# Kernel tuning notes

Measured on AMD Instinct MI355X. Metric: run time of the kernel, lower is better.

The kernel has to match this reference:

```python
import jax, jax.numpy as jnp
import numpy as np

N_HEAD = 16
D_HEAD = 64
D_LATENT = 32
BLOCK_SIZE = 2048


def rope_cache(dim, max_seq_len, theta=10000.0):
    inv_freq = 1.0 / (theta ** (jnp.arange(0, dim, 2, dtype=jnp.float32) / dim))
    t = jnp.arange(max_seq_len, dtype=jnp.float32)
    freqs = jnp.einsum('i,j->ij', t, inv_freq)        # [T, dim/2]
    emb = jnp.concatenate([freqs, freqs], axis=-1)    # [T, dim]
    return jnp.cos(emb), jnp.sin(emb)


def apply_rope(x, cos, sin):
    # x: [B, H, T, C]; interleaved-pair rotation as in the torch module
    B, H, T, C = x.shape
    c = cos[:T][None, None]
    s = sin[:T][None, None]
    x1 = x[..., 0::2]
    x2 = x[..., 1::2]
    rotated = jnp.stack((-x2, x1), axis=-1).reshape(B, H, T, C)
    return x * c + rotated * s


def setup_inputs() -> dict:
    key = jax.random.key(0)
    ks = jax.random.split(key, 7)
    sd = 0.02
    return {
        'x':   jax.random.normal(ks[0], (2, 2048, 1024), dtype=jnp.float32),
        'Wq':  jax.random.normal(ks[1], (1024, 1024), dtype=jnp.float32) * sd,
        'Wk':  jax.random.normal(ks[2], (512, 1024), dtype=jnp.float32) * sd,
        'Wv':  jax.random.normal(ks[3], (512, 1024), dtype=jnp.float32) * sd,
        'Wku': jax.random.normal(ks[4], (64, 32), dtype=jnp.float32) * sd,
        'Wvu': jax.random.normal(ks[5], (64, 32), dtype=jnp.float32) * sd,
        'Wc':  jax.random.normal(ks[6], (1024, 1024), dtype=jnp.float32) * sd,
    }


def reference(x, Wq, Wk, Wv, Wku, Wvu, Wc):
    B, T, C = x.shape
    H, Dh, Dl = N_HEAD, D_HEAD, D_LATENT

    # latent KV (compressed cache entries)
    k_lat = (x @ Wk.T).reshape(B, T, H, Dl)   # [B,T,H,Dl]
    v_lat = (x @ Wv.T).reshape(B, T, H, Dl)

    # q and up-projected k/v -> [B,H,T,Dh]
    q = (x @ Wq.T).reshape(B, T, H, Dh).transpose(0, 2, 1, 3)
    k = jnp.einsum('bthl,dl->bhtd', k_lat, Wku)
    v = jnp.einsum('bthl,dl->bhtd', v_lat, Wvu)

    cos, sin = rope_cache(Dh, BLOCK_SIZE)
    q = apply_rope(q, cos, sin)
    k = apply_rope(k, cos, sin)

    scale = 1.0 / jnp.sqrt(jnp.asarray(Dh, dtype=x.dtype))
    att = jnp.einsum('bhqd,bhkd->bhqk', q, k) * scale   # [B,H,T,T]
    causal = jnp.tril(jnp.ones((T, T), dtype=bool))
    att = jnp.where(causal[None, None], att, -jnp.inf)
    att = jax.nn.softmax(att, axis=-1)

    y = jnp.einsum('bhqk,bhkd->bhqd', att, v)           # [B,H,T,Dh]
    y = y.transpose(0, 2, 1, 3).reshape(B, T, C) @ Wc.T  # [B,T,C]
    return y, k_lat, v_lat
```

## Files before the change

kernel.cpp:

```cpp
#include <hip/hip_runtime.h>
#include <math.h>

#define NHEAD  16
#define DHEAD  64
#define DLAT   32
#define TSEQ   2048
#define NBATCH 2
#define CDIM   1024
#define MROWS  (NBATCH*TSEQ)

typedef __attribute__((ext_vector_type(8))) short bf16x8;
typedef __attribute__((ext_vector_type(4))) short bf16x4;
typedef __attribute__((ext_vector_type(4))) float f32x4;

#define AS1 __attribute__((address_space(1)))
#define AS3 __attribute__((address_space(3)))

__device__ __forceinline__ unsigned short f2bf(float f) {
    union { float f; unsigned u; } v; v.f = f;
    unsigned r = v.u + 0x7fff + ((v.u >> 16) & 1);
    return (unsigned short)(r >> 16);
}

__device__ __forceinline__ unsigned pk2(float lo, float hi) {
    return (unsigned)f2bf(lo) | ((unsigned)f2bf(hi) << 16);
}

__device__ __forceinline__ unsigned pack_trunc(float hi, float lo) {
    return __builtin_amdgcn_perm(__float_as_uint(hi), __float_as_uint(lo), 0x07060302u);
}

__device__ __forceinline__ void gld_lds16(const unsigned short* g, unsigned short* l) {
    __builtin_amdgcn_global_load_lds((const AS1 void*)g, (AS3 void*)l, 16, 0, 0);
}

__device__ __forceinline__ f32x4 mfma_16x16x16_bf16(bf16x4 a, bf16x4 b, f32x4 c) {
#if __has_builtin(__builtin_amdgcn_mfma_f32_16x16x16bf16_1k)
    return __builtin_amdgcn_mfma_f32_16x16x16bf16_1k(a, b, c, 0, 0, 0);
#else
    asm volatile("v_mfma_f32_16x16x16_bf16 %0, %1, %2, %0\n\ts_nop 4"
                 : "+v"(c) : "v"(a), "v"(b));
    return c;
#endif
}

__global__ __launch_bounds__(256) void cvt_all(
        const float* __restrict__ x,  const float* __restrict__ wq,
        const float* __restrict__ wk, const float* __restrict__ wv,
        const float* __restrict__ wc, const float* __restrict__ wku,
        const float* __restrict__ wvu,
        unsigned short* __restrict__ xb, unsigned short* __restrict__ wall) {
    int i = (blockIdx.x * 256 + threadIdx.x) * 4;
    const float* src; unsigned short* dst; int off;
    if      (i < 4194304) { src = x;   dst = xb;             off = 0;       }
    else if (i < 5242880) { src = wq;  dst = wall;           off = 4194304; }
    else if (i < 5767168) { src = wk;  dst = wall + 1048576; off = 5242880; }
    else if (i < 6291456) { src = wv;  dst = wall + 1572864; off = 5767168; }
    else if (i < 7340032) { src = wc;  dst = wall + 2097152; off = 6291456; }
    else if (i < 7342080) { src = wku; dst = wall + 3145728; off = 7340032; }
    else                  { src = wvu; dst = wall + 3147776; off = 7342080; }
    float4 v = *(const float4*)(src + (i - off));
    ushort4 o = { f2bf(v.x), f2bf(v.y), f2bf(v.z), f2bf(v.w) };
    *(ushort4*)(dst + (i - off)) = o;
}

__device__ __forceinline__ void gemm_core(
        const unsigned short* __restrict__ A, const unsigned short* __restrict__ W,
        int K, int bm, int bn, unsigned short* As, unsigned short* Bs,
        f32x4 (&acc)[4][4]) {
    const int tid = threadIdx.x;
    const int w = tid >> 6, lane = tid & 63;
    const int quad = lane >> 4, l16 = lane & 15;
    const int wm = (w >> 1) * 64, wn = (w & 1) * 64;

    const int lr = lane >> 2;
    const int le = (lane & 3) * 8;
    const unsigned short* Ag0 = A + (size_t)(bm + w*32 + lr) * K + le;
    const unsigned short* Wg0 = W + (size_t)(bn + w*32 + lr) * K + le;
    unsigned short* AsD0 = &As[(w*32 +  0) * 32];
    unsigned short* AsD1 = &As[(w*32 + 16) * 32];
    unsigned short* BsD0 = &Bs[(w*32 +  0) * 32];
    unsigned short* BsD1 = &Bs[(w*32 + 16) * 32];

    for (int k0 = 0; k0 < K; k0 += 32) {
        gld_lds16(Ag0 + k0,                AsD0);
        gld_lds16(Ag0 + k0 + (size_t)16*K, AsD1);
        gld_lds16(Wg0 + k0,                BsD0);
        gld_lds16(Wg0 + k0 + (size_t)16*K, BsD1);
        __syncthreads();
        bf16x8 af[4], bf[4];
        #pragma unroll
        for (int t = 0; t < 4; ++t)
            af[t] = *(const bf16x8*)&As[(wm + t*16 + l16)*32 + quad*8];
        #pragma unroll
        for (int c = 0; c < 4; ++c)
            bf[c] = *(const bf16x8*)&Bs[(wn + c*16 + l16)*32 + quad*8];
        #pragma unroll
        for (int t = 0; t < 4; ++t)
            #pragma unroll
            for (int c = 0; c < 4; ++c)
                acc[t][c] = __builtin_amdgcn_mfma_f32_16x16x32_bf16(af[t], bf[c], acc[t][c], 0, 0, 0);
        __syncthreads();
    }
}

__global__ __launch_bounds__(256) void gemm_proj(
        const unsigned short* __restrict__ A, const unsigned short* __restrict__ W,
        float* __restrict__ qproj, float* __restrict__ okl, float* __restrict__ ovl,
        int K) {
    __shared__ unsigned short As[128*32];
    __shared__ unsigned short Bs[128*32];
    const int bm = blockIdx.y * 128, bn = blockIdx.x * 128;
    f32x4 acc[4][4] = {};
    gemm_core(A, W, K, bm, bn, As, Bs, acc);

    const int tid = threadIdx.x;
    const int w = tid >> 6, lane = tid & 63;
    const int quad = lane >> 4, l16 = lane & 15;
    const int wm = (w >> 1) * 64, wn = (w & 1) * 64;

    float* base; int ldo;
    if (bn < 1024)      { base = qproj + bn;        ldo = 1024; }
    else if (bn < 1536) { base = okl + (bn - 1024); ldo = 512;  }
    else                { base = ovl + (bn - 1536); ldo = 512;  }

    #pragma unroll
    for (int t = 0; t < 4; ++t)
        #pragma unroll
        for (int c = 0; c < 4; ++c)
            #pragma unroll
            for (int r = 0; r < 4; ++r) {
                int row = bm + wm + t*16 + quad*4 + r;
                int col = wn + c*16 + l16;
                base[(size_t)row * ldo + col] = acc[t][c][r];
            }
}

__global__ __launch_bounds__(256) void gemm_out(
        const unsigned short* __restrict__ A, const unsigned short* __restrict__ W,
        float* __restrict__ O, int N, int K) {
    __shared__ unsigned short As[128*32];
    __shared__ unsigned short Bs[128*32];
    const int bm = blockIdx.y * 128, bn = blockIdx.x * 128;
    f32x4 acc[4][4] = {};
    gemm_core(A, W, K, bm, bn, As, Bs, acc);

    const int tid = threadIdx.x;
    const int w = tid >> 6, lane = tid & 63;
    const int quad = lane >> 4, l16 = lane & 15;
    const int wm = (w >> 1) * 64, wn = (w & 1) * 64;
    #pragma unroll
    for (int t = 0; t < 4; ++t)
        #pragma unroll
        for (int c = 0; c < 4; ++c)
            #pragma unroll
            for (int r = 0; r < 4; ++r) {
                int row = bm + wm + t*16 + quad*4 + r;
                int col = bn + wn + c*16 + l16;
                O[(size_t)row * N + col] = acc[t][c][r];
            }
}

#define QSCALE 0.18033688011112042f
__global__ __launch_bounds__(256) void latup(
        const float* __restrict__ qproj, const float* __restrict__ klat,
        const float* __restrict__ vlat,
        const unsigned short* __restrict__ wkub, const unsigned short* __restrict__ wvub,
        unsigned short* __restrict__ qb, unsigned short* __restrict__ kb,
        unsigned short* __restrict__ vt) {
    __shared__ __attribute__((aligned(16))) unsigned short ksh[4][16][72];
    __shared__ __attribute__((aligned(16))) unsigned short qsh[4][16][72];
    __shared__ __attribute__((aligned(16))) unsigned short vsh[4][64][24];

    const int bh = blockIdx.y, b = bh >> 4, h = bh & 15;
    const int tid = threadIdx.x, w = tid >> 6, lane = tid & 63;
    const int quad = lane >> 4, l16 = lane & 15;
    const int tw = blockIdx.x * 64 + w * 16;
    const int t  = tw + l16;

    const float* klp = klat + ((size_t)(b*TSEQ + t))*(NHEAD*DLAT) + h*DLAT + quad*8;
    const float* vlp = vlat + ((size_t)(b*TSEQ + t))*(NHEAD*DLAT) + h*DLAT + quad*8;
    float4 kA = *(const float4*)klp, kB = *(const float4*)(klp + 4);
    float4 vA = *(const float4*)vlp, vB = *(const float4*)(vlp + 4);

    bf16x8 xk[4], xv[4];
    #pragma unroll
    for (int c = 0; c < 4; ++c) {
        xk[c] = *(const bf16x8*)&wkub[(c*16 + l16)*DLAT + quad*8];
        xv[c] = *(const bf16x8*)&wvub[(c*16 + l16)*DLAT + quad*8];
    }

    union { bf16x8 v; unsigned u[4]; } yk, yv;
    yk.u[0] = pk2(kA.x, kA.y); yk.u[1] = pk2(kA.z, kA.w);
    yk.u[2] = pk2(kB.x, kB.y); yk.u[3] = pk2(kB.z, kB.w);
    yv.u[0] = pk2(vA.x, vA.y); yv.u[1] = pk2(vA.z, vA.w);
    yv.u[2] = pk2(vB.x, vB.y); yv.u[3] = pk2(vB.z, vB.w);

    f32x4 aK[4], aV[4];
    #pragma unroll
    for (int c = 0; c < 4; ++c) {
        f32x4 z = {0.f, 0.f, 0.f, 0.f};
        aK[c] = __builtin_amdgcn_mfma_f32_16x16x32_bf16(xk[c], yk.v, z, 0, 0, 0);
        aV[c] = __builtin_amdgcn_mfma_f32_16x16x32_bf16(xv[c], yv.v, z, 0, 0, 0);
    }

    float C0[4], S0[4], C1[4], S1[4];
    const float tf = (float)t;
    #pragma unroll
    for (int j = 0; j < 4; ++j) {
        float f0 = (float)(quad*4 + j);
        __sincosf(tf * __expf(-f0 * 0.28782313662425572f),          &S0[j], &C0[j]);
        __sincosf(tf * __expf(-(f0 + 16.f) * 0.28782313662425572f), &S1[j], &C1[j]);
    }

    const float* qrow = qproj + ((size_t)(b*TSEQ + t))*CDIM + h*DHEAD;
    #pragma unroll
    for (int c = 0; c < 4; ++c) {
        const float* Cs = (c & 1) ? C1 : C0;
        const float* Ss = (c & 1) ? S1 : S0;
        float a0 = aK[c][0], a1 = aK[c][1], a2 = aK[c][2], a3 = aK[c][3];
        unsigned kw0 = pk2(a0*Cs[0] - a1*Ss[0], a1*Cs[1] + a0*Ss[1]);
        unsigned kw1 = pk2(a2*Cs[2] - a3*Ss[2], a3*Cs[3] + a2*Ss[3]);
        *(uint2*)&ksh[w][l16][c*16 + quad*4] = make_uint2(kw0, kw1);

        float4 qv = *(const float4*)(qrow + c*16 + quad*4);
        unsigned qw0 = pk2((qv.x*Cs[0] - qv.y*Ss[0])*QSCALE, (qv.y*Cs[1] + qv.x*Ss[1])*QSCALE);
        unsigned qw1 = pk2((qv.z*Cs[2] - qv.w*Ss[2])*QSCALE, (qv.w*Cs[3] + qv.z*Ss[3])*QSCALE);
        *(uint2*)&qsh[w][l16][c*16 + quad*4] = make_uint2(qw0, qw1);

        vsh[w][c*16 + quad*4 + 0][l16] = f2bf(aV[c][0]);
        vsh[w][c*16 + quad*4 + 1][l16] = f2bf(aV[c][1]);
        vsh[w][c*16 + quad*4 + 2][l16] = f2bf(aV[c][2]);
        vsh[w][c*16 + quad*4 + 3][l16] = f2bf(aV[c][3]);
    }

    __asm__ __volatile__("s_waitcnt lgkmcnt(0)" ::: "memory");

    const int ro = lane >> 2, co = (lane & 3) * 16;
    size_t go = ((size_t)bh*TSEQ + tw + ro)*DHEAD + co;
    int4 k0o = *(const int4*)&ksh[w][ro][co];
    int4 k1o = *(const int4*)&ksh[w][ro][co + 8];
    *(int4*)&kb[go]     = k0o;
    *(int4*)&kb[go + 8] = k1o;
    int4 q0o = *(const int4*)&qsh[w][ro][co];
    int4 q1o = *(const int4*)&qsh[w][ro][co + 8];
    *(int4*)&qb[go]     = q0o;
    *(int4*)&qb[go + 8] = q1o;

    size_t vo = ((size_t)bh*DHEAD + lane)*TSEQ + tw;
    int4 v0o = *(const int4*)&vsh[w][lane][0];
    int4 v1o = *(const int4*)&vsh[w][lane][8];
    *(int4*)&vt[vo]     = v0o;
    *(int4*)&vt[vo + 8] = v1o;
}

__global__ __launch_bounds__(256, 2) void flash_attn(
        const unsigned short* __restrict__ qb, const unsigned short* __restrict__ kb,
        const unsigned short* __restrict__ vtb, unsigned short* __restrict__ yatt) {
    const int bh = blockIdx.x;
    const int b = bh >> 4, h = bh & 15;

    __shared__ unsigned short Ks[2][128][64];
    __shared__ unsigned short VTs[2][64][128];

    const int tid  = threadIdx.x;
    const int wq   = tid >> 6;
    const int lane = tid & 63;
    const int quad = lane >> 4;
    const int l16  = lane & 15;

    const unsigned short* Kbase = kb  + (size_t)bh * TSEQ * DHEAD;
    const unsigned short* Vbase = vtb + (size_t)bh * DHEAD * TSEQ;

    const int kr8 = lane >> 3, kcp = lane & 7;
    const int kcl = (kcp ^ kr8) * 8;
    const int vr4 = lane >> 4, vcp = lane & 15;

    const int kx0 = (quad ^ (l16 & 7)) * 8;
    const int kx1 = ((quad + 4) ^ (l16 & 7)) * 8;
    const int vq = (quad >> 1), vodd = (quad & 1) * 4;

    for (int half = 0; half < 2; ++half) {
        const int qt = half ? (31 - (int)blockIdx.y) : (int)blockIdx.y;
        const int n128 = (qt + 2) >> 1;

        const unsigned short* qbase =
            qb + ((size_t)bh*TSEQ + qt*64 + wq*16 + l16) * DHEAD + quad*8;
        bf16x8 qB0 = *(const bf16x8*)qbase;
        bf16x8 qB1 = *(const bf16x8*)(qbase + 32);

        f32x4 oacc[4] = {};
        float m_run = -1e30f, l_run = 0.f;

        __syncthreads();
        #pragma unroll
        for (int i = 0; i < 4; ++i) {
            gld_lds16(Kbase + (size_t)(wq*32 + i*8 + kr8)*DHEAD + kcl,
                      &Ks[0][wq*32 + i*8][0]);
            int vcl = (vcp ^ ((i*4 + vr4) & 15)) * 8;
            gld_lds16(Vbase + (size_t)(wq*16 + i*4 + vr4)*TSEQ + vcl,
                      &VTs[0][wq*16 + i*4][0]);
        }
        __syncthreads();

        for (int j = 0; j < n128; ++j) {
            const int buf = j & 1;
            if (j + 1 < n128) {
                const int kc = (j + 1) * 128;
                #pragma unroll
                for (int i = 0; i < 4; ++i) {
                    gld_lds16(Kbase + (size_t)(kc + wq*32 + i*8 + kr8)*DHEAD + kcl,
                              &Ks[buf^1][wq*32 + i*8][0]);
                    int vcl = (vcp ^ ((i*4 + vr4) & 15)) * 8;
                    gld_lds16(Vbase + (size_t)(wq*16 + i*4 + vr4)*TSEQ + kc + vcl,
                              &VTs[buf^1][wq*16 + i*4][0]);
                }
            }

            f32x4 sacc[8];
            __builtin_amdgcn_s_setprio(1);
            #pragma unroll
            for (int c = 0; c < 8; ++c) {
                bf16x8 ak0 = *(const bf16x8*)&Ks[buf][c*16 + l16][kx0];
                bf16x8 ak1 = *(const bf16x8*)&Ks[buf][c*16 + l16][kx1];
                f32x4 z = {0.f, 0.f, 0.f, 0.f};
                z = __builtin_amdgcn_mfma_f32_16x16x32_bf16(ak0, qB0, z, 0, 0, 0);
                z = __builtin_amdgcn_mfma_f32_16x16x32_bf16(ak1, qB1, z, 0, 0, 0);
                sacc[c] = z;
            }
            __builtin_amdgcn_s_setprio(0);
            if (j == n128 - 1) {
                #pragma unroll
                for (int c = 0; c < 8; ++c)
                    #pragma unroll
                    for (int r = 0; r < 4; ++r)
                        if (j*128 + c*16 + quad*4 + r > qt*64 + wq*16 + l16)
                            sacc[c][r] = -1e30f;
            }

            float mx = -1e30f;
            #pragma unroll
            for (int c = 0; c < 8; ++c)
                #pragma unroll
                for (int r = 0; r < 4; ++r) mx = fmaxf(mx, sacc[c][r]);
            mx = fmaxf(mx, __shfl_xor(mx, 16, 64));
            mx = fmaxf(mx, __shfl_xor(mx, 32, 64));
            if (!__all(mx <= m_run + 8.f)) {
                float mn = fmaxf(m_run, mx);
                float alpha = __builtin_exp2f(m_run - mn);
                m_run = mn;
                l_run *= alpha;
                #pragma unroll
                for (int c = 0; c < 4; ++c)
                    #pragma unroll
                    for (int r = 0; r < 4; ++r) oacc[c][r] *= alpha;
            }
            float ls = 0.f;
            #pragma unroll
            for (int c = 0; c < 8; ++c)
                #pragma unroll
                for (int r = 0; r < 4; ++r) {
                    float p = __builtin_exp2f(sacc[c][r] - m_run);
                    sacc[c][r] = p;
                    ls += p;
                }
            ls += __shfl_xor(ls, 16, 64);
            ls += __shfl_xor(ls, 32, 64);
            l_run += ls;

            __builtin_amdgcn_s_setprio(1);
            #pragma unroll
            for (int c = 0; c < 8; ++c) {
                union { bf16x4 v; unsigned u[2]; } bP;
                bP.u[0] = pack_trunc(sacc[c][1], sacc[c][0]);
                bP.u[1] = pack_trunc(sacc[c][3], sacc[c][2]);
                const int vcol = ((2*c + vq) ^ l16) * 8 + vodd;
                #pragma unroll
                for (int dc = 0; dc < 4; ++dc) {
                    bf16x4 av = *(const bf16x4*)&VTs[buf][dc*16 + l16][vcol];
                    oacc[dc] = mfma_16x16x16_bf16(av, bP.v, oacc[dc]);
                }
            }
            __builtin_amdgcn_s_setprio(0);

            __syncthreads();
        }

        float invl = 1.0f / l_run;
        unsigned short* Wt = &Ks[0][0][0] + wq * (16*72);
        #pragma unroll
        for (int c = 0; c < 4; ++c)
            #pragma unroll
            for (int r = 0; r < 4; ++r)
                Wt[(size_t)l16*72 + c*16 + quad*4 + r] = f2bf(oacc[c][r] * invl);
        __asm__ __volatile__("" ::: "memory");
        #pragma unroll
        for (int p = 0; p < 2; ++p) {
            int row = p*8 + (lane >> 3);
            int d0 = (lane & 7) * 8;
            int4 val = *(const int4*)&Wt[row*72 + d0];
            int tg = qt*64 + wq*16 + row;
            *(int4*)&yatt[((size_t)(b*TSEQ + tg))*CDIM + h*DHEAD + d0] = val;
        }
    }
}

extern "C" void kernel_launch(void* const* d_in, const int* in_sizes, int n_in,
                              void* d_out, int out_size, void* d_ws, size_t ws_size,
                              hipStream_t stream) {
    const float* x   = (const float*)d_in[0];
    const float* Wq  = (const float*)d_in[1];
    const float* Wk  = (const float*)d_in[2];
    const float* Wv  = (const float*)d_in[3];
    const float* Wku = (const float*)d_in[4];
    const float* Wvu = (const float*)d_in[5];
    const float* Wc  = (const float*)d_in[6];

    float* out_y  = (float*)d_out;
    float* out_kl = out_y  + (size_t)MROWS * CDIM;
    float* out_vl = out_kl + (size_t)MROWS * NHEAD*DLAT;

    float* qproj = (float*)d_ws;
    unsigned short* xb   = (unsigned short*)(qproj + (size_t)MROWS*CDIM);
    unsigned short* qb   = xb  + (size_t)MROWS*CDIM;
    unsigned short* kb   = qb  + (size_t)MROWS*CDIM;
    unsigned short* vt   = kb  + (size_t)MROWS*CDIM;
    unsigned short* wall = vt  + (size_t)MROWS*CDIM;
    unsigned short* wcb  = wall + (size_t)2048*CDIM;
    unsigned short* wkub = wall + 3145728;
    unsigned short* wvub = wall + 3147776;
    unsigned short* yatt = (unsigned short*)qproj;

    cvt_all<<<7172, 256, 0, stream>>>(x, Wq, Wk, Wv, Wc, Wku, Wvu, xb, wall);

    gemm_proj<<<dim3(2048/128, MROWS/128), 256, 0, stream>>>(
        xb, wall, qproj, out_kl, out_vl, CDIM);

    latup<<<dim3(TSEQ/64, NBATCH*NHEAD), 256, 0, stream>>>(
        qproj, out_kl, out_vl, wkub, wvub, qb, kb, vt);

    flash_attn<<<dim3(NBATCH*NHEAD, 16), 256, 0, stream>>>(qb, kb, vt, yatt);

    gemm_out<<<dim3(CDIM/128, MROWS/128), 256, 0, stream>>>(yatt, wcb, out_y, CDIM, CDIM);
}
```

Before: 206.9 us.

## Process both paired query tiles in one K/V pass to share loads

Instead of running the light and heavy query tiles one after the other, each with its own K/V streaming loop, the kernel now keeps two sets of accumulators and streams K/V once for the longer tile. The shorter tile also computes against each block while it is still active. This halves K/V global-to-LDS traffic and the LDS reads of K and V for the overlapping range, and removes one loop's worth of barriers. In exchange it doubles the accumulator and score registers, which may pressure occupancy at launch bounds of 2 blocks per SM.

```diff
diff --git a/kernel.cpp b/kernel.cpp
--- a/kernel.cpp
+++ b/kernel.cpp
@@ -254,6 +254,39 @@
     *(int4*)&vt[vo + 8] = v1o;
 }
 
+__device__ __forceinline__ void online_sm(f32x4 (&s)[8], float& m_run, float& l_run,
+                                          f32x4 (&o)[4]) {
+    float mx = -1e30f;
+    #pragma unroll
+    for (int c = 0; c < 8; ++c)
+        #pragma unroll
+        for (int r = 0; r < 4; ++r) mx = fmaxf(mx, s[c][r]);
+    mx = fmaxf(mx, __shfl_xor(mx, 16, 64));
+    mx = fmaxf(mx, __shfl_xor(mx, 32, 64));
+    if (!__all(mx <= m_run + 8.f)) {
+        float mn = fmaxf(m_run, mx);
+        float alpha = __builtin_exp2f(m_run - mn);
+        m_run = mn;
+        l_run *= alpha;
+        #pragma unroll
+        for (int c = 0; c < 4; ++c)
+            #pragma unroll
+            for (int r = 0; r < 4; ++r) o[c][r] *= alpha;
+    }
+    float ls = 0.f;
+    #pragma unroll
+    for (int c = 0; c < 8; ++c)
+        #pragma unroll
+        for (int r = 0; r < 4; ++r) {
+            float p = __builtin_exp2f(s[c][r] - m_run);
+            s[c][r] = p;
+            ls += p;
+        }
+    ls += __shfl_xor(ls, 16, 64);
+    ls += __shfl_xor(ls, 32, 64);
+    l_run += ls;
+}
+
 __global__ __launch_bounds__(256, 2) void flash_attn(
         const unsigned short* __restrict__ qb, const unsigned short* __restrict__ kb,
         const unsigned short* __restrict__ vtb, unsigned short* __restrict__ yatt) {
@@ -280,119 +313,145 @@
     const int kx1 = ((quad + 4) ^ (l16 & 7)) * 8;
     const int vq = (quad >> 1), vodd = (quad & 1) * 4;
 
-    for (int half = 0; half < 2; ++half) {
-        const int qt = half ? (31 - (int)blockIdx.y) : (int)blockIdx.y;
-        const int n128 = (qt + 2) >> 1;
-
-        const unsigned short* qbase =
-            qb + ((size_t)bh*TSEQ + qt*64 + wq*16 + l16) * DHEAD + quad*8;
-        bf16x8 qB0 = *(const bf16x8*)qbase;
-        bf16x8 qB1 = *(const bf16x8*)(qbase + 32);
-
-        f32x4 oacc[4] = {};
-        float m_run = -1e30f, l_run = 0.f;
-
-        __syncthreads();
-        #pragma unroll
-        for (int i = 0; i < 4; ++i) {
-            gld_lds16(Kbase + (size_t)(wq*32 + i*8 + kr8)*DHEAD + kcl,
-                      &Ks[0][wq*32 + i*8][0]);
-            int vcl = (vcp ^ ((i*4 + vr4) & 15)) * 8;
-            gld_lds16(Vbase + (size_t)(wq*16 + i*4 + vr4)*TSEQ + vcl,
-                      &VTs[0][wq*16 + i*4][0]);
-        }
-        __syncthreads();
-
-        for (int j = 0; j < n128; ++j) {
-            const int buf = j & 1;
-            if (j + 1 < n128) {
-                const int kc = (j + 1) * 128;
-                #pragma unroll
-                for (int i = 0; i < 4; ++i) {
-                    gld_lds16(Kbase + (size_t)(kc + wq*32 + i*8 + kr8)*DHEAD + kcl,
-                              &Ks[buf^1][wq*32 + i*8][0]);
-                    int vcl = (vcp ^ ((i*4 + vr4) & 15)) * 8;
-                    gld_lds16(Vbase + (size_t)(wq*16 + i*4 + vr4)*TSEQ + kc + vcl,
-                              &VTs[buf^1][wq*16 + i*4][0]);
-                }
-            }
-
-            f32x4 sacc[8];
-            __builtin_amdgcn_s_setprio(1);
+    const int qtA = blockIdx.y;
+    const int qtB = 31 - qtA;
+    const int nA  = (qtA + 2) >> 1;
+    const int nB  = (qtB + 2) >> 1;
+
+    const unsigned short* qbaseA =
+        qb + ((size_t)bh*TSEQ + qtA*64 + wq*16 + l16) * DHEAD + quad*8;
+    const unsigned short* qbaseB =
+        qb + ((size_t)bh*TSEQ + qtB*64 + wq*16 + l16) * DHEAD + quad*8;
+    bf16x8 qA0 = *(const bf16x8*)qbaseA;
+    bf16x8 qA1 = *(const bf16x8*)(qbaseA + 32);
+    bf16x8 qB0 = *(const bf16x8*)qbaseB;
+    bf16x8 qB1 = *(const bf16x8*)(qbaseB + 32);
+
+    f32x4 oA[4] = {}, oB[4] = {};
+    float mA = -1e30f, lA = 0.f;
+    float mB = -1e30f, lB = 0.f;
+
+    #pragma unroll
+    for (int i = 0; i < 4; ++i) {
+        gld_lds16(Kbase + (size_t)(wq*32 + i*8 + kr8)*DHEAD + kcl,
+                  &Ks[0][wq*32 + i*8][0]);
+        int vcl = (vcp ^ ((i*4 + vr4) & 15)) * 8;
+        gld_lds16(Vbase + (size_t)(wq*16 + i*4 + vr4)*TSEQ + vcl,
+                  &VTs[0][wq*16 + i*4][0]);
+    }
+    __syncthreads();
+
+    for (int j = 0; j < nB; ++j) {
+        const int buf = j & 1;
+        if (j + 1 < nB) {
+            const int kc = (j + 1) * 128;
+            #pragma unroll
+            for (int i = 0; i < 4; ++i) {
+                gld_lds16(Kbase + (size_t)(kc + wq*32 + i*8 + kr8)*DHEAD + kcl,
+                          &Ks[buf^1][wq*32 + i*8][0]);
+                int vcl = (vcp ^ ((i*4 + vr4) & 15)) * 8;
+                gld_lds16(Vbase + (size_t)(wq*16 + i*4 + vr4)*TSEQ + kc + vcl,
+                          &VTs[buf^1][wq*16 + i*4][0]);
+            }
+        }
+        const bool actA = (j < nA);
+
+        f32x4 sA[8], sB[8];
+        __builtin_amdgcn_s_setprio(1);
+        if (actA) {
             #pragma unroll
             for (int c = 0; c < 8; ++c) {
                 bf16x8 ak0 = *(const bf16x8*)&Ks[buf][c*16 + l16][kx0];
                 bf16x8 ak1 = *(const bf16x8*)&Ks[buf][c*16 + l16][kx1];
-                f32x4 z = {0.f, 0.f, 0.f, 0.f};
-                z = __builtin_amdgcn_mfma_f32_16x16x32_bf16(ak0, qB0, z, 0, 0, 0);
-                z = __builtin_amdgcn_mfma_f32_16x16x32_bf16(ak1, qB1, z, 0, 0, 0);
-                sacc[c] = z;
-            }
-            __builtin_amdgcn_s_setprio(0);
-            if (j == n128 - 1) {
-                #pragma unroll
-                for (int c = 0; c < 8; ++c)
-                    #pragma unroll
-                    for (int r = 0; r < 4; ++r)
-                        if (j*128 + c*16 + quad*4 + r > qt*64 + wq*16 + l16)
-                            sacc[c][r] = -1e30f;
-            }
-
-            float mx = -1e30f;
+                f32x4 zB = {0.f, 0.f, 0.f, 0.f};
+                zB = __builtin_amdgcn_mfma_f32_16x16x32_bf16(ak0, qB0, zB, 0, 0, 0);
+                zB = __builtin_amdgcn_mfma_f32_16x16x32_bf16(ak1, qB1, zB, 0, 0, 0);
+                sB[c] = zB;
+                f32x4 zA = {0.f, 0.f, 0.f, 0.f};
+                zA = __builtin_amdgcn_mfma_f32_16x16x32_bf16(ak0, qA0, zA, 0, 0, 0);
+                zA = __builtin_amdgcn_mfma_f32_16x16x32_bf16(ak1, qA1, zA, 0, 0, 0);
+                sA[c] = zA;
+            }
+        } else {
+            #pragma unroll
+            for (int c = 0; c < 8; ++c) {
+                bf16x8 ak0 = *(const bf16x8*)&Ks[buf][c*16 + l16][kx0];
+                bf16x8 ak1 = *(const bf16x8*)&Ks[buf][c*16 + l16][kx1];
+                f32x4 zB = {0.f, 0.f, 0.f, 0.f};
+                zB = __builtin_amdgcn_mfma_f32_16x16x32_bf16(ak0, qB0, zB, 0, 0, 0);
+                zB = __builtin_amdgcn_mfma_f32_16x16x32_bf16(ak1, qB1, zB, 0, 0, 0);
+                sB[c] = zB;
+            }
+        }
+        __builtin_amdgcn_s_setprio(0);
+
+        if (j == nB - 1) {
             #pragma unroll
             for (int c = 0; c < 8; ++c)
                 #pragma unroll
-                for (int r = 0; r < 4; ++r) mx = fmaxf(mx, sacc[c][r]);
-            mx = fmaxf(mx, __shfl_xor(mx, 16, 64));
-            mx = fmaxf(mx, __shfl_xor(mx, 32, 64));
-            if (!__all(mx <= m_run + 8.f)) {
-                float mn = fmaxf(m_run, mx);
-                float alpha = __builtin_exp2f(m_run - mn);
-                m_run = mn;
-                l_run *= alpha;
-                #pragma unroll
-                for (int c = 0; c < 4; ++c)
-                    #pragma unroll
-                    for (int r = 0; r < 4; ++r) oacc[c][r] *= alpha;
-            }
-            float ls = 0.f;
+                for (int r = 0; r < 4; ++r)
+                    if (j*128 + c*16 + quad*4 + r > qtB*64 + wq*16 + l16)
+                        sB[c][r] = -1e30f;
+        }
+        if (actA && j == nA - 1) {
             #pragma unroll
             for (int c = 0; c < 8; ++c)
                 #pragma unroll
-                for (int r = 0; r < 4; ++r) {
-                    float p = __builtin_exp2f(sacc[c][r] - m_run);
-                    sacc[c][r] = p;
-                    ls += p;
-                }
-            ls += __shfl_xor(ls, 16, 64);
-            ls += __shfl_xor(ls, 32, 64);
-            l_run += ls;
-
-            __builtin_amdgcn_s_setprio(1);
+                for (int r = 0; r < 4; ++r)
+                    if (j*128 + c*16 + quad*4 + r > qtA*64 + wq*16 + l16)
+                        sA[c][r] = -1e30f;
+        }
+
+        online_sm(sB, mB, lB, oB);
+        if (actA) online_sm(sA, mA, lA, oA);
+
+        __builtin_amdgcn_s_setprio(1);
+        if (actA) {
             #pragma unroll
             for (int c = 0; c < 8; ++c) {
-                union { bf16x4 v; unsigned u[2]; } bP;
-                bP.u[0] = pack_trunc(sacc[c][1], sacc[c][0]);
-                bP.u[1] = pack_trunc(sacc[c][3], sacc[c][2]);
+                union { bf16x4 v; unsigned u[2]; } bPB, bPA;
+                bPB.u[0] = pack_trunc(sB[c][1], sB[c][0]);
+                bPB.u[1] = pack_trunc(sB[c][3], sB[c][2]);
+                bPA.u[0] = pack_trunc(sA[c][1], sA[c][0]);
+                bPA.u[1] = pack_trunc(sA[c][3], sA[c][2]);
                 const int vcol = ((2*c + vq) ^ l16) * 8 + vodd;
                 #pragma unroll
                 for (int dc = 0; dc < 4; ++dc) {
                     bf16x4 av = *(const bf16x4*)&VTs[buf][dc*16 + l16][vcol];
-                    oacc[dc] = mfma_16x16x16_bf16(av, bP.v, oacc[dc]);
+                    oB[dc] = mfma_16x16x16_bf16(av, bPB.v, oB[dc]);
+                    oA[dc] = mfma_16x16x16_bf16(av, bPA.v, oA[dc]);
                 }
             }
-            __builtin_amdgcn_s_setprio(0);
-
-            __syncthreads();
-        }
-
-        float invl = 1.0f / l_run;
-        unsigned short* Wt = &Ks[0][0][0] + wq * (16*72);
+        } else {
+            #pragma unroll
+            for (int c = 0; c < 8; ++c) {
+                union { bf16x4 v; unsigned u[2]; } bPB;
+                bPB.u[0] = pack_trunc(sB[c][1], sB[c][0]);
+                bPB.u[1] = pack_trunc(sB[c][3], sB[c][2]);
+                const int vcol = ((2*c + vq) ^ l16) * 8 + vodd;
+                #pragma unroll
+                for (int dc = 0; dc < 4; ++dc) {
+                    bf16x4 av = *(const bf16x4*)&VTs[buf][dc*16 + l16][vcol];
+                    oB[dc] = mfma_16x16x16_bf16(av, bPB.v, oB[dc]);
+                }
+            }
+        }
+        __builtin_amdgcn_s_setprio(0);
+
+        __syncthreads();
+    }
+
+    #pragma unroll
+    for (int half = 0; half < 2; ++half) {
+        const f32x4* o = half ? oB : oA;
+        float invl = 1.0f / (half ? lB : lA);
+        int qt = half ? qtB : qtA;
+        unsigned short* Wt = &Ks[half][0][0] + wq * (16*72);
         #pragma unroll
         for (int c = 0; c < 4; ++c)
             #pragma unroll
             for (int r = 0; r < 4; ++r)
-                Wt[(size_t)l16*72 + c*16 + quad*4 + r] = f2bf(oacc[c][r] * invl);
+                Wt[(size_t)l16*72 + c*16 + quad*4 + r] = f2bf(o[c][r] * invl);
         __asm__ __volatile__("" ::: "memory");
         #pragma unroll
         for (int p = 0; p < 2; ++p) {
```

After: 204.2 us. No clear change (-1.3%).

## Use 512-thread GEMM blocks and one-query-tile-per-block flash attention with 64-key tiles

Applied to the files above, without the earlier changes.

The GEMM kernels now run eight waves per 128x128 tile, each computing a 64x32 subtile, so per-thread accumulators halve and more waves hide latency. Flash attention drops the paired-half scheme: each block handles a single 64-row query tile, and tiles are issued largest-first by reversing blockIdx.y. The grid doubles to 32 tiles per head, key/value tiles shrink to 64 with smaller LDS, and launch bounds allow 4 blocks per CU. The aim is more occupancy and finer load balancing, at the cost of more loop iterations and barriers, and of relying on the scheduler instead of static pairing to balance the causal triangle.

```diff
diff --git a/kernel.cpp b/kernel.cpp
--- a/kernel.cpp
+++ b/kernel.cpp
@@ -67,57 +67,53 @@
 __device__ __forceinline__ void gemm_core(
         const unsigned short* __restrict__ A, const unsigned short* __restrict__ W,
         int K, int bm, int bn, unsigned short* As, unsigned short* Bs,
-        f32x4 (&acc)[4][4]) {
+        f32x4 (&acc)[4][2]) {
     const int tid = threadIdx.x;
     const int w = tid >> 6, lane = tid & 63;
     const int quad = lane >> 4, l16 = lane & 15;
-    const int wm = (w >> 1) * 64, wn = (w & 1) * 64;
-
-    const int lr = lane >> 2;
-    const int le = (lane & 3) * 8;
-    const unsigned short* Ag0 = A + (size_t)(bm + w*32 + lr) * K + le;
-    const unsigned short* Wg0 = W + (size_t)(bn + w*32 + lr) * K + le;
-    unsigned short* AsD0 = &As[(w*32 +  0) * 32];
-    unsigned short* AsD1 = &As[(w*32 + 16) * 32];
-    unsigned short* BsD0 = &Bs[(w*32 +  0) * 32];
-    unsigned short* BsD1 = &Bs[(w*32 + 16) * 32];
+    const int wm = (w >> 2) * 64, wn = (w & 3) * 32;
+
+    const int sr = tid >> 2;
+    const int sc = (tid & 3) * 8;
+    const unsigned short* Ag0 = A + (size_t)(bm + sr) * K + sc;
+    const unsigned short* Wg0 = W + (size_t)(bn + sr) * K + sc;
+    unsigned short* AsD = &As[(w*16) * 32];
+    unsigned short* BsD = &Bs[(w*16) * 32];
 
     for (int k0 = 0; k0 < K; k0 += 32) {
-        gld_lds16(Ag0 + k0,                AsD0);
-        gld_lds16(Ag0 + k0 + (size_t)16*K, AsD1);
-        gld_lds16(Wg0 + k0,                BsD0);
-        gld_lds16(Wg0 + k0 + (size_t)16*K, BsD1);
+        gld_lds16(Ag0 + k0, AsD);
+        gld_lds16(Wg0 + k0, BsD);
         __syncthreads();
-        bf16x8 af[4], bf[4];
+        bf16x8 af[4], bf[2];
         #pragma unroll
         for (int t = 0; t < 4; ++t)
             af[t] = *(const bf16x8*)&As[(wm + t*16 + l16)*32 + quad*8];
         #pragma unroll
-        for (int c = 0; c < 4; ++c)
+        for (int c = 0; c < 2; ++c)
             bf[c] = *(const bf16x8*)&Bs[(wn + c*16 + l16)*32 + quad*8];
         #pragma unroll
         for (int t = 0; t < 4; ++t)
             #pragma unroll
-            for (int c = 0; c < 4; ++c)
+            for (int c = 0; c < 2; ++c)
                 acc[t][c] = __builtin_amdgcn_mfma_f32_16x16x32_bf16(af[t], bf[c], acc[t][c], 0, 0, 0);
         __syncthreads();
     }
 }
 
-__global__ __launch_bounds__(256) void gemm_proj(
+__global__ __launch_bounds__(512) void gemm_proj(
         const unsigned short* __restrict__ A, const unsigned short* __restrict__ W,
         float* __restrict__ qproj, float* __restrict__ okl, float* __restrict__ ovl,
         int K) {
     __shared__ unsigned short As[128*32];
     __shared__ unsigned short Bs[128*32];
     const int bm = blockIdx.y * 128, bn = blockIdx.x * 128;
-    f32x4 acc[4][4] = {};
+    f32x4 acc[4][2] = {};
     gemm_core(A, W, K, bm, bn, As, Bs, acc);
 
     const int tid = threadIdx.x;
     const int w = tid >> 6, lane = tid & 63;
     const int quad = lane >> 4, l16 = lane & 15;
-    const int wm = (w >> 1) * 64, wn = (w & 1) * 64;
+    const int wm = (w >> 2) * 64, wn = (w & 3) * 32;
 
     float* base; int ldo;
     if (bn < 1024)      { base = qproj + bn;        ldo = 1024; }
@@ -127,7 +123,7 @@
     #pragma unroll
     for (int t = 0; t < 4; ++t)
         #pragma unroll
-        for (int c = 0; c < 4; ++c)
+        for (int c = 0; c < 2; ++c)
             #pragma unroll
             for (int r = 0; r < 4; ++r) {
                 int row = bm + wm + t*16 + quad*4 + r;
@@ -136,23 +132,23 @@
             }
 }
 
-__global__ __launch_bounds__(256) void gemm_out(
+__global__ __launch_bounds__(512) void gemm_out(
         const unsigned short* __restrict__ A, const unsigned short* __restrict__ W,
         float* __restrict__ O, int N, int K) {
     __shared__ unsigned short As[128*32];
     __shared__ unsigned short Bs[128*32];
     const int bm = blockIdx.y * 128, bn = blockIdx.x * 128;
-    f32x4 acc[4][4] = {};
+    f32x4 acc[4][2] = {};
     gemm_core(A, W, K, bm, bn, As, Bs, acc);
 
     const int tid = threadIdx.x;
     const int w = tid >> 6, lane = tid & 63;
     const int quad = lane >> 4, l16 = lane & 15;
-    const int wm = (w >> 1) * 64, wn = (w & 1) * 64;
+    const int wm = (w >> 2) * 64, wn = (w & 3) * 32;
     #pragma unroll
     for (int t = 0; t < 4; ++t)
         #pragma unroll
-        for (int c = 0; c < 4; ++c)
+        for (int c = 0; c < 2; ++c)
             #pragma unroll
             for (int r = 0; r < 4; ++r) {
                 int row = bm + wm + t*16 + quad*4 + r;
@@ -254,14 +250,15 @@
     *(int4*)&vt[vo + 8] = v1o;
 }
 
-__global__ __launch_bounds__(256, 2) void flash_attn(
+__global__ __launch_bounds__(256, 4) void flash_attn(
         const unsigned short* __restrict__ qb, const unsigned short* __restrict__ kb,
         const unsigned short* __restrict__ vtb, unsigned short* __restrict__ yatt) {
     const int bh = blockIdx.x;
+    const int qt = 31 - (int)blockIdx.y;
     const int b = bh >> 4, h = bh & 15;
 
-    __shared__ unsigned short Ks[2][128][64];
-    __shared__ unsigned short VTs[2][64][128];
+    __shared__ unsigned short Ks[2][64][64];
+    __shared__ unsigned short VTs[2][64][64];
 
     const int tid  = threadIdx.x;
     const int wq   = tid >> 6;
@@ -272,136 +269,131 @@
     const unsigned short* Kbase = kb  + (size_t)bh * TSEQ * DHEAD;
     const unsigned short* Vbase = vtb + (size_t)bh * DHEAD * TSEQ;
 
-    const int kr8 = lane >> 3, kcp = lane & 7;
-    const int kcl = (kcp ^ kr8) * 8;
-    const int vr4 = lane >> 4, vcp = lane & 15;
+    const int r8  = lane >> 3;
+    const int c8  = lane & 7;
+    const int scl = (c8 ^ r8) * 8;
 
     const int kx0 = (quad ^ (l16 & 7)) * 8;
     const int kx1 = ((quad + 4) ^ (l16 & 7)) * 8;
     const int vq = (quad >> 1), vodd = (quad & 1) * 4;
 
-    for (int half = 0; half < 2; ++half) {
-        const int qt = half ? (31 - (int)blockIdx.y) : (int)blockIdx.y;
-        const int n128 = (qt + 2) >> 1;
-
-        const unsigned short* qbase =
-            qb + ((size_t)bh*TSEQ + qt*64 + wq*16 + l16) * DHEAD + quad*8;
-        bf16x8 qB0 = *(const bf16x8*)qbase;
-        bf16x8 qB1 = *(const bf16x8*)(qbase + 32);
-
-        f32x4 oacc[4] = {};
-        float m_run = -1e30f, l_run = 0.f;
+    const int n64 = qt + 1;
+
+    const unsigned short* qbase =
+        qb + ((size_t)bh*TSEQ + qt*64 + wq*16 + l16) * DHEAD + quad*8;
+    bf16x8 q0 = *(const bf16x8*)qbase;
+    bf16x8 q1 = *(const bf16x8*)(qbase + 32);
+
+    f32x4 oacc[4] = {};
+    float m_run = -1e30f, l_run = 0.f;
+
+    #pragma unroll
+    for (int i = 0; i < 2; ++i) {
+        gld_lds16(Kbase + (size_t)(wq*16 + i*8 + r8)*DHEAD + scl,
+                  &Ks[0][wq*16 + i*8][0]);
+        gld_lds16(Vbase + (size_t)(wq*16 + i*8 + r8)*TSEQ + scl,
+                  &VTs[0][wq*16 + i*8][0]);
+    }
+    __syncthreads();
+
+    for (int j = 0; j < n64; ++j) {
+        const int buf = j & 1;
+        if (j + 1 < n64) {
+            const int kc = (j + 1) * 64;
+            #pragma unroll
+            for (int i = 0; i < 2; ++i) {
+                gld_lds16(Kbase + (size_t)(kc + wq*16 + i*8 + r8)*DHEAD + scl,
+                          &Ks[buf^1][wq*16 + i*8][0]);
+                gld_lds16(Vbase + (size_t)(wq*16 + i*8 + r8)*TSEQ + kc + scl,
+                          &VTs[buf^1][wq*16 + i*8][0]);
+            }
+        }
+
+        f32x4 s[4];
+        __builtin_amdgcn_s_setprio(1);
+        #pragma unroll
+        for (int c = 0; c < 4; ++c) {
+            bf16x8 ak0 = *(const bf16x8*)&Ks[buf][c*16 + l16][kx0];
+            bf16x8 ak1 = *(const bf16x8*)&Ks[buf][c*16 + l16][kx1];
+            f32x4 z = {0.f, 0.f, 0.f, 0.f};
+            z = __builtin_amdgcn_mfma_f32_16x16x32_bf16(ak0, q0, z, 0, 0, 0);
+            z = __builtin_amdgcn_mfma_f32_16x16x32_bf16(ak1, q1, z, 0, 0, 0);
+            s[c] = z;
+        }
+        __builtin_amdgcn_s_setprio(0);
+
+        if (j == n64 - 1) {
+            #pragma unroll
+            for (int c = 0; c < 4; ++c)
+                #pragma unroll
+                for (int r = 0; r < 4; ++r)
+                    if (c*16 + quad*4 + r > wq*16 + l16)
+                        s[c][r] = -1e30f;
+        }
+
+        float mx = -1e30f;
+        #pragma unroll
+        for (int c = 0; c < 4; ++c)
+            #pragma unroll
+            for (int r = 0; r < 4; ++r) mx = fmaxf(mx, s[c][r]);
+        mx = fmaxf(mx, __shfl_xor(mx, 16, 64));
+        mx = fmaxf(mx, __shfl_xor(mx, 32, 64));
+        if (!__all(mx <= m_run + 8.f)) {
+            float mn = fmaxf(m_run, mx);
+            float alpha = __builtin_exp2f(m_run - mn);
+            m_run = mn;
+            l_run *= alpha;
+            #pragma unroll
+            for (int c = 0; c < 4; ++c)
+                #pragma unroll
+                for (int r = 0; r < 4; ++r) oacc[c][r] *= alpha;
+        }
+        float ls = 0.f;
+        #pragma unroll
+        for (int c = 0; c < 4; ++c)
+            #pragma unroll
+            for (int r = 0; r < 4; ++r) {
+                float p = __builtin_exp2f(s[c][r] - m_run);
+                s[c][r] = p;
+                ls += p;
+            }
+        ls += __shfl_xor(ls, 16, 64);
+        ls += __shfl_xor(ls, 32, 64);
+        l_run += ls;
+
+        __builtin_amdgcn_s_setprio(1);
+        #pragma unroll
+        for (int c = 0; c < 4; ++c) {
+            union { bf16x4 v; unsigned u[2]; } bP;
+            bP.u[0] = pack_trunc(s[c][1], s[c][0]);
+            bP.u[1] = pack_trunc(s[c][3], s[c][2]);
+            const int vcol = ((2*c + vq) ^ (l16 & 7)) * 8 + vodd;
+            #pragma unroll
+            for (int dc = 0; dc < 4; ++dc) {
+                bf16x4 av = *(const bf16x4*)&VTs[buf][dc*16 + l16][vcol];
+                oacc[dc] = mfma_16x16x16_bf16(av, bP.v, oacc[dc]);
+            }
+        }
+        __builtin_amdgcn_s_setprio(0);
 
         __syncthreads();
-        #pragma unroll
-        for (int i = 0; i < 4; ++i) {
-            gld_lds16(Kbase + (size_t)(wq*32 + i*8 + kr8)*DHEAD + kcl,
-                      &Ks[0][wq*32 + i*8][0]);
-            int vcl = (vcp ^ ((i*4 + vr4) & 15)) * 8;
-            gld_lds16(Vbase + (size_t)(wq*16 + i*4 + vr4)*TSEQ + vcl,
-                      &VTs[0][wq*16 + i*4][0]);
-        }
-        __syncthreads();
-
-        for (int j = 0; j < n128; ++j) {
-            const int buf = j & 1;
-            if (j + 1 < n128) {
-                const int kc = (j + 1) * 128;
-                #pragma unroll
-                for (int i = 0; i < 4; ++i) {
-                    gld_lds16(Kbase + (size_t)(kc + wq*32 + i*8 + kr8)*DHEAD + kcl,
-                              &Ks[buf^1][wq*32 + i*8][0]);
-                    int vcl = (vcp ^ ((i*4 + vr4) & 15)) * 8;
-                    gld_lds16(Vbase + (size_t)(wq*16 + i*4 + vr4)*TSEQ + kc + vcl,
-                              &VTs[buf^1][wq*16 + i*4][0]);
-                }
-            }
-
-            f32x4 sacc[8];
-            __builtin_amdgcn_s_setprio(1);
-            #pragma unroll
-            for (int c = 0; c < 8; ++c) {
-                bf16x8 ak0 = *(const bf16x8*)&Ks[buf][c*16 + l16][kx0];
-                bf16x8 ak1 = *(const bf16x8*)&Ks[buf][c*16 + l16][kx1];
-                f32x4 z = {0.f, 0.f, 0.f, 0.f};
-                z = __builtin_amdgcn_mfma_f32_16x16x32_bf16(ak0, qB0, z, 0, 0, 0);
-                z = __builtin_amdgcn_mfma_f32_16x16x32_bf16(ak1, qB1, z, 0, 0, 0);
-                sacc[c] = z;
-            }
-            __builtin_amdgcn_s_setprio(0);
-            if (j == n128 - 1) {
-                #pragma unroll
-                for (int c = 0; c < 8; ++c)
-                    #pragma unroll
-                    for (int r = 0; r < 4; ++r)
-                        if (j*128 + c*16 + quad*4 + r > qt*64 + wq*16 + l16)
-                            sacc[c][r] = -1e30f;
-            }
-
-            float mx = -1e30f;
-            #pragma unroll
-            for (int c = 0; c < 8; ++c)
-                #pragma unroll
-                for (int r = 0; r < 4; ++r) mx = fmaxf(mx, sacc[c][r]);
-            mx = fmaxf(mx, __shfl_xor(mx, 16, 64));
-            mx = fmaxf(mx, __shfl_xor(mx, 32, 64));
-            if (!__all(mx <= m_run + 8.f)) {
-                float mn = fmaxf(m_run, mx);
-                float alpha = __builtin_exp2f(m_run - mn);
-                m_run = mn;
-                l_run *= alpha;
-                #pragma unroll
-                for (int c = 0; c < 4; ++c)
-                    #pragma unroll
-                    for (int r = 0; r < 4; ++r) oacc[c][r] *= alpha;
-            }
-            float ls = 0.f;
-            #pragma unroll
-            for (int c = 0; c < 8; ++c)
-                #pragma unroll
-                for (int r = 0; r < 4; ++r) {
-                    float p = __builtin_exp2f(sacc[c][r] - m_run);
-                    sacc[c][r] = p;
-                    ls += p;
-                }
-            ls += __shfl_xor(ls, 16, 64);
-            ls += __shfl_xor(ls, 32, 64);
-            l_run += ls;
-
-            __builtin_amdgcn_s_setprio(1);
-            #pragma unroll
-            for (int c = 0; c < 8; ++c) {
-                union { bf16x4 v; unsigned u[2]; } bP;
-                bP.u[0] = pack_trunc(sacc[c][1], sacc[c][0]);
-                bP.u[1] = pack_trunc(sacc[c][3], sacc[c][2]);
-                const int vcol = ((2*c + vq) ^ l16) * 8 + vodd;
-                #pragma unroll
-                for (int dc = 0; dc < 4; ++dc) {
-                    bf16x4 av = *(const bf16x4*)&VTs[buf][dc*16 + l16][vcol];
-                    oacc[dc] = mfma_16x16x16_bf16(av, bP.v, oacc[dc]);
-                }
-            }
-            __builtin_amdgcn_s_setprio(0);
-
-            __syncthreads();
-        }
-
-        float invl = 1.0f / l_run;
-        unsigned short* Wt = &Ks[0][0][0] + wq * (16*72);
-        #pragma unroll
-        for (int c = 0; c < 4; ++c)
-            #pragma unroll
-            for (int r = 0; r < 4; ++r)
-                Wt[(size_t)l16*72 + c*16 + quad*4 + r] = f2bf(oacc[c][r] * invl);
-        __asm__ __volatile__("" ::: "memory");
-        #pragma unroll
-        for (int p = 0; p < 2; ++p) {
-            int row = p*8 + (lane >> 3);
-            int d0 = (lane & 7) * 8;
-            int4 val = *(const int4*)&Wt[row*72 + d0];
-            int tg = qt*64 + wq*16 + row;
-            *(int4*)&yatt[((size_t)(b*TSEQ + tg))*CDIM + h*DHEAD + d0] = val;
-        }
+    }
+
+    float invl = 1.0f / l_run;
+    unsigned short* Wt = &Ks[0][0][0] + wq * (16*72);
+    #pragma unroll
+    for (int c = 0; c < 4; ++c)
+        #pragma unroll
+        for (int r = 0; r < 4; ++r)
+            Wt[(size_t)l16*72 + c*16 + quad*4 + r] = f2bf(oacc[c][r] * invl);
+    __asm__ __volatile__("" ::: "memory");
+    #pragma unroll
+    for (int p = 0; p < 2; ++p) {
+        int row = p*8 + (lane >> 3);
+        int d0 = (lane & 7) * 8;
+        int4 val = *(const int4*)&Wt[row*72 + d0];
+        int tg = qt*64 + wq*16 + row;
+        *(int4*)&yatt[((size_t)(b*TSEQ + tg))*CDIM + h*DHEAD + d0] = val;
     }
 }
 
@@ -433,13 +425,13 @@
 
     cvt_all<<<7172, 256, 0, stream>>>(x, Wq, Wk, Wv, Wc, Wku, Wvu, xb, wall);
 
-    gemm_proj<<<dim3(2048/128, MROWS/128), 256, 0, stream>>>(
+    gemm_proj<<<dim3(2048/128, MROWS/128), 512, 0, stream>>>(
         xb, wall, qproj, out_kl, out_vl, CDIM);
 
     latup<<<dim3(TSEQ/64, NBATCH*NHEAD), 256, 0, stream>>>(
         qproj, out_kl, out_vl, wkub, wvub, qb, kb, vt);
 
-    flash_attn<<<dim3(NBATCH*NHEAD, 16), 256, 0, stream>>>(qb, kb, vt, yatt);
-
-    gemm_out<<<dim3(CDIM/128, MROWS/128), 256, 0, stream>>>(yatt, wcb, out_y, CDIM, CDIM);
-}
+    flash_attn<<<dim3(NBATCH*NHEAD, 32), 256, 0, stream>>>(qb, kb, vt, yatt);
+
+    gemm_out<<<dim3(CDIM/128, MROWS/128), 512, 0, stream>>>(yatt, wcb, out_y, CDIM, CDIM);
+}
```

New measurement: 200.3 us. -3.2%, faster.
